# Kernel optimization log

Hardware: AMD Instinct MI355X
Metric: run time of the kernel (lower is better)

The kernel has to match this reference:

```python
import jax, jax.numpy as jnp
import numpy as np

IMG_H, IMG_W = 4096, 4096
CELL_H, CELL_W = 8, 8
N_BINS = 9
DELTA = 180.0 / N_BINS
EPS = 1e-9


def setup_inputs() -> dict:
    key = jax.random.key(0)
    x = jax.random.uniform(key, (1, 3, IMG_H, IMG_W), dtype=jnp.float32)
    return {"x": x}


def reference(x):
    # conv kernels are [1,3,3,3] with identical 3x3 per input channel -> equivalent
    # to summing channels first then applying the 3x3 stencil (zero padding=1).
    s = x.sum(axis=1)                      # [B, H, W]
    sp = jnp.pad(s, ((0, 0), (1, 1), (1, 1)))
    g_v = sp[:, 2:, 1:-1] - sp[:, :-2, 1:-1]   # vertical gradient
    g_h = sp[:, 1:-1, 2:] - sp[:, 1:-1, :-2]   # horizontal gradient
    mag = jnp.sqrt(g_v ** 2 + g_h ** 2 + 1e-6)
    ang = jnp.abs(jnp.arctan(g_h / (g_v + EPS)) * (180.0 / np.pi))  # in [0, 90]

    mag2 = mag[0]  # B==1: squeeze -> [H, W]
    ang2 = ang[0]

    # Bug-faithful replication of hists(): `bins` is re-created per pixel and
    # only the LAST pixel of each cell survives in temp.append(bins).
    pm = mag2[CELL_H - 1::CELL_H, CELL_W - 1::CELL_W]  # [nH, nW]
    pa = ang2[CELL_H - 1::CELL_H, CELL_W - 1::CELL_W]

    j = jnp.floor(pa / DELTA - 0.5)         # jth_bin; can be -1 (Python neg-index wrap)
    c_j1 = DELTA * (j + 1.5)                # jth_bin_centre(j+1)
    v_j = pm * ((c_j1 - pa) / DELTA)        # jth_bin_value
    v_j1 = pm - v_j

    ji = j.astype(jnp.int32)
    idx0 = jnp.mod(ji, N_BINS)              # replicates bins[-1] wraparound
    idx1 = jnp.mod(ji + 1, N_BINS)
    oh0 = jax.nn.one_hot(idx0, N_BINS, dtype=pm.dtype)
    oh1 = jax.nn.one_hot(idx1, N_BINS, dtype=pm.dtype)
    hist = v_j[..., None] * oh0 + v_j1[..., None] * oh1  # [nH, nW, N_BINS]

    # features(): 2x2 blocks of cells, stride 1, flattened row-major, L2-normalized
    blk = jnp.concatenate(
        [hist[:-1, :-1], hist[:-1, 1:], hist[1:, :-1], hist[1:, 1:]], axis=-1
    )  # [nH-1, nW-1, 4*N_BINS]
    norm = jnp.sqrt(jnp.sum(blk ** 2, axis=-1, keepdims=True))
    feat = blk / (norm + EPS)
    return feat
```

## Files before the change

### kernel.cpp

```cpp
#include <hip/hip_runtime.h>
#include <math.h>


#define IMG 4096
#define CSTRIDE (4096 * 4096)
#define NCELL 512
#define NOUT 511
#define TS 16
#define HT 17

__device__ __forceinline__ float load_s(const float* __restrict__ x, int y, int xx) {
    size_t idx = (size_t)y * IMG + xx;
    return (x[idx] + x[idx + CSTRIDE]) + x[idx + 2 * (size_t)CSTRIDE];
}

__device__ __forceinline__ void hist9(const float* __restrict__ x, int gr, int gc,
                                      float* __restrict__ out ) {
    const int y = 8 * gr + 7;
    const int xx = 8 * gc + 7;
    const float s_up = load_s(x, y - 1, xx);
    const float s_dn = (y + 1 < IMG) ? load_s(x, y + 1, xx) : 0.0f;
    const float s_lf = load_s(x, y, xx - 1);
    const float s_rt = (xx + 1 < IMG) ? load_s(x, y, xx + 1) : 0.0f;

    const float g_v = s_dn - s_up;
    const float g_h = s_rt - s_lf;

    const float mag = sqrtf(g_v * g_v + g_h * g_h + 1e-6f);
    const float ang = fabsf(atanf(g_h / (g_v + 1e-9f)) * 57.29577951308232f);

    const float jf = floorf(ang / 20.0f - 0.5f);
    const float vj = mag * ((20.0f * (jf + 1.5f) - ang) / 20.0f);
    const float vj1 = mag - vj;
    const int ji = (int)jf;
    const int i0 = (ji + 9) % 9;
    const int i1 = (i0 + 1) % 9;

#pragma unroll
    for (int b = 0; b < 9; ++b) out[b] = 0.0f;
    out[i0] = vj;
    out[i1] = vj1;
}

__global__ __launch_bounds__(256) void hog_kernel(const float* __restrict__ x,
                                                  float* __restrict__ out) {
    __shared__ float hist[HT * HT * 9];

    const int bi = blockIdx.y;
    const int bj = blockIdx.x;
    const int tid = threadIdx.x;

    for (int e = tid; e < HT * HT; e += 256) {
        const int r = e / HT;
        const int c = e % HT;
        int gr = bi * TS + r; if (gr > NCELL - 1) gr = NCELL - 1;
        int gc = bj * TS + c; if (gc > NCELL - 1) gc = NCELL - 1;
        hist9(x, gr, gc, &hist[e * 9]);
    }
    __syncthreads();

    const int ty = tid >> 4;
    const int tx = tid & 15;
    const int oi = bi * TS + ty;
    const int oj = bj * TS + tx;
    if (oi >= NOUT || oj >= NOUT) return;

    const float* h00 = &hist[((ty    ) * HT + tx    ) * 9];
    const float* h01 = &hist[((ty    ) * HT + tx + 1) * 9];
    const float* h10 = &hist[((ty + 1) * HT + tx    ) * 9];
    const float* h11 = &hist[((ty + 1) * HT + tx + 1) * 9];

    float v[36];
#pragma unroll
    for (int b = 0; b < 9; ++b) {
        v[b]      = h00[b];
        v[9 + b]  = h01[b];
        v[18 + b] = h10[b];
        v[27 + b] = h11[b];
    }
    float ss = 0.0f;
#pragma unroll
    for (int c = 0; c < 36; ++c) ss += v[c] * v[c];
    const float inv = 1.0f / (sqrtf(ss) + 1e-9f);

    float* o = out + ((size_t)oi * NOUT + oj) * 36;
#pragma unroll
    for (int c = 0; c < 36; ++c) o[c] = v[c] * inv;
}

extern "C" void kernel_launch(void* const* d_in, const int* in_sizes, int n_in,
                              void* d_out, int out_size, void* d_ws, size_t ws_size,
                              hipStream_t stream) {
    (void)in_sizes; (void)n_in; (void)d_ws; (void)ws_size; (void)out_size;
    const float* x = (const float*)d_in[0];
    float* out = (float*)d_out;

    dim3 grid((NOUT + TS - 1) / TS, (NOUT + TS - 1) / TS);
    dim3 block(256);
    hipLaunchKernelGGL(hog_kernel, grid, block, 0, stream, x, out);
}
```

Baseline: 261.0 us.

## Stage needed image rows in LDS with float4 loads and split output writes

The kernel now cooperatively loads the three image rows around each cell's sample pixel into shared memory with vectorized float4 loads, summing the channels as it goes. Stencil taps are then read from LDS instead of being fetched as scattered scalar global loads per cell. The normalization stage is spread across 4 threads per output, each handling 9 bins, with a shuffle reduction for the norm so that output stores are more coalesced. This loads many unused columns (full 128-wide row spans) in exchange for contiguous access, and it adds LDS usage and an extra barrier.

```diff
diff --git a/kernel.cpp b/kernel.cpp
--- a/kernel.cpp
+++ b/kernel.cpp
@@ -4,88 +4,92 @@
 
 #define IMG 4096
 #define CSTRIDE (4096 * 4096)
-#define NCELL 512
 #define NOUT 511
 #define TS 16
 #define HT 17
-
-__device__ __forceinline__ float load_s(const float* __restrict__ x, int y, int xx) {
-    size_t idx = (size_t)y * IMG + xx;
-    return (x[idx] + x[idx + CSTRIDE]) + x[idx + 2 * (size_t)CSTRIDE];
-}
-
-__device__ __forceinline__ void hist9(const float* __restrict__ x, int gr, int gc,
-                                      float* __restrict__ out ) {
-    const int y = 8 * gr + 7;
-    const int xx = 8 * gc + 7;
-    const float s_up = load_s(x, y - 1, xx);
-    const float s_dn = (y + 1 < IMG) ? load_s(x, y + 1, xx) : 0.0f;
-    const float s_lf = load_s(x, y, xx - 1);
-    const float s_rt = (xx + 1 < IMG) ? load_s(x, y, xx + 1) : 0.0f;
-
-    const float g_v = s_dn - s_up;
-    const float g_h = s_rt - s_lf;
-
-    const float mag = sqrtf(g_v * g_v + g_h * g_h + 1e-6f);
-    const float ang = fabsf(atanf(g_h / (g_v + 1e-9f)) * 57.29577951308232f);
-
-    const float jf = floorf(ang / 20.0f - 0.5f);
-    const float vj = mag * ((20.0f * (jf + 1.5f) - ang) / 20.0f);
-    const float vj1 = mag - vj;
-    const int ji = (int)jf;
-    const int i0 = (ji + 9) % 9;
-    const int i1 = (i0 + 1) % 9;
-
-#pragma unroll
-    for (int b = 0; b < 9; ++b) out[b] = 0.0f;
-    out[i0] = vj;
-    out[i1] = vj1;
-}
+#define NROWS 51
+#define NQ 34
+#define RS 136
 
 __global__ __launch_bounds__(256) void hog_kernel(const float* __restrict__ x,
                                                   float* __restrict__ out) {
+    __shared__ float raw[NROWS * RS];
     __shared__ float hist[HT * HT * 9];
 
-    const int bi = blockIdx.y;
-    const int bj = blockIdx.x;
-    const int tid = threadIdx.x;
+    const int bi = blockIdx.y, bj = blockIdx.x, tid = threadIdx.x;
+    const int col0 = 128 * bj + 4;
 
-    for (int e = tid; e < HT * HT; e += 256) {
-        const int r = e / HT;
-        const int c = e % HT;
-        int gr = bi * TS + r; if (gr > NCELL - 1) gr = NCELL - 1;
-        int gc = bj * TS + c; if (gc > NCELL - 1) gc = NCELL - 1;
-        hist9(x, gr, gc, &hist[e * 9]);
+    for (int t = tid; t < NROWS * NQ; t += 256) {
+        const int rr = t / NQ;
+        const int q  = t - rr * NQ;
+        const int r  = rr / 3;
+        const int dt = rr - 3 * r;
+        const int y  = 128 * bi + 8 * r + 6 + dt;
+        const int gc = col0 + 4 * q;
+        float4 v = make_float4(0.f, 0.f, 0.f, 0.f);
+        if (y < IMG && gc + 3 < IMG) {
+            const size_t base = (size_t)y * IMG + gc;
+            const float4 a = *(const float4*)(x + base);
+            const float4 b = *(const float4*)(x + base + (size_t)CSTRIDE);
+            const float4 c = *(const float4*)(x + base + 2 * (size_t)CSTRIDE);
+            v.x = (a.x + b.x) + c.x;
+            v.y = (a.y + b.y) + c.y;
+            v.z = (a.z + b.z) + c.z;
+            v.w = (a.w + b.w) + c.w;
+        }
+        *(float4*)&raw[rr * RS + 4 * q] = v;
     }
     __syncthreads();
 
-    const int ty = tid >> 4;
-    const int tx = tid & 15;
-    const int oi = bi * TS + ty;
-    const int oj = bj * TS + tx;
-    if (oi >= NOUT || oj >= NOUT) return;
+    for (int cell = tid; cell < HT * HT; cell += 256) {
+        const int r = cell / HT;
+        const int k = cell - r * HT;
+        const float s_up = raw[(3 * r    ) * RS + 8 * k + 3];
+        const float s_lf = raw[(3 * r + 1) * RS + 8 * k + 2];
+        const float s_rt = raw[(3 * r + 1) * RS + 8 * k + 4];
+        const float s_dn = raw[(3 * r + 2) * RS + 8 * k + 3];
 
-    const float* h00 = &hist[((ty    ) * HT + tx    ) * 9];
-    const float* h01 = &hist[((ty    ) * HT + tx + 1) * 9];
-    const float* h10 = &hist[((ty + 1) * HT + tx    ) * 9];
-    const float* h11 = &hist[((ty + 1) * HT + tx + 1) * 9];
+        const float g_v = s_dn - s_up;
+        const float g_h = s_rt - s_lf;
+        const float mag = sqrtf(g_v * g_v + g_h * g_h + 1e-6f);
+        const float ang = fabsf(atanf(g_h / (g_v + 1e-9f)) * 57.29577951308232f);
+        const float jf  = floorf(ang * 0.05f - 0.5f);
+        const float vj  = mag * ((20.0f * (jf + 1.5f) - ang) * 0.05f);
+        const float vj1 = mag - vj;
+        int i0 = (int)jf; if (i0 < 0) i0 += 9;
+        const int i1 = (i0 == 8) ? 0 : i0 + 1;
 
-    float v[36];
+        float* h = &hist[cell * 9];
 #pragma unroll
-    for (int b = 0; b < 9; ++b) {
-        v[b]      = h00[b];
-        v[9 + b]  = h01[b];
-        v[18 + b] = h10[b];
-        v[27 + b] = h11[b];
+        for (int b = 0; b < 9; ++b)
+            h[b] = (b == i0) ? vj : ((b == i1) ? vj1 : 0.0f);
     }
-    float ss = 0.0f;
+    __syncthreads();
+
+    const int p  = tid & 3;
+    const int c0 = tid >> 2;
+    for (int it = 0; it < 4; ++it) {
+        const int cell = it * 64 + c0;
+        const int ty = cell >> 4;
+        const int tx = cell & 15;
+        const int hr = ty + (p >> 1);
+        const int hc = tx + (p & 1);
+        const float* h = &hist[(hr * HT + hc) * 9];
+        float v[9];
+        float ss = 0.f;
 #pragma unroll
-    for (int c = 0; c < 36; ++c) ss += v[c] * v[c];
-    const float inv = 1.0f / (sqrtf(ss) + 1e-9f);
-
-    float* o = out + ((size_t)oi * NOUT + oj) * 36;
+        for (int b = 0; b < 9; ++b) { v[b] = h[b]; ss += v[b] * v[b]; }
+        ss += __shfl_xor(ss, 1);
+        ss += __shfl_xor(ss, 2);
+        const int oi = 16 * bi + ty;
+        const int oj = 16 * bj + tx;
+        if (oi < NOUT && oj < NOUT) {
+            const float inv = 1.0f / (sqrtf(ss) + 1e-9f);
+            float* o = out + ((size_t)oi * NOUT + oj) * 36 + p * 9;
 #pragma unroll
-    for (int c = 0; c < 36; ++c) o[c] = v[c] * inv;
+            for (int b = 0; b < 9; ++b) o[b] = v[b] * inv;
+        }
+    }
 }
 
 extern "C" void kernel_launch(void* const* d_in, const int* in_sizes, int n_in,
@@ -94,8 +98,7 @@
     (void)in_sizes; (void)n_in; (void)d_ws; (void)ws_size; (void)out_size;
     const float* x = (const float*)d_in[0];
     float* out = (float*)d_out;
-
-    dim3 grid((NOUT + TS - 1) / TS, (NOUT + TS - 1) / TS);
+    dim3 grid(32, 32);
     dim3 block(256);
     hipLaunchKernelGGL(hog_kernel, grid, block, 0, stream, x, out);
 }
```

After: 255.6 us. -2.0%, faster.
